# Kernel tuning notes

Measured on AMD Instinct MI355X. Metric: run time of the kernel, lower is better.

## Reference

```python
import jax, jax.numpy as jnp
import numpy as np

L = 8       # num decoder layers
S = 192     # seq_len = h*w = 24*8
D = 512     # d_model
DFF = 2048  # dim_feedforward
H, W, BS = 24, 8, 16
EPS = 1e-5


def setup_inputs() -> dict:
    key = jax.random.key(0)
    ks = jax.random.split(key, 8)
    f = jax.random.normal
    return {
        "q_feat": f(ks[0], (BS, D * L, H, W), jnp.float32),
        "g_feat": f(ks[1], (BS, D * L, H, W), jnp.float32),
        "targets": jax.random.randint(ks[2], (BS,), 0, 8),
        "score_embed": f(ks[3], (L, S, S), jnp.float32) * 0.05,
        "fc0_w": f(ks[4], (L, D, D), jnp.float32) * (1.0 / np.sqrt(D)),
        "fc0_b": jnp.zeros((L, D), jnp.float32),
        "bn1_g": jnp.ones((L,), jnp.float32),
        "bn1_b": jnp.zeros((L,), jnp.float32),
        "fc2_w": f(ks[5], (L, DFF, S), jnp.float32) * (1.0 / np.sqrt(S)),
        "fc2_b": jnp.zeros((L, DFF), jnp.float32),
        "bn2_g": jnp.ones((L, DFF), jnp.float32),
        "bn2_b": jnp.zeros((L, DFF), jnp.float32),
        "fc3_w": f(ks[6], (L, DFF), jnp.float32) * (1.0 / np.sqrt(DFF)),
        "fc3_b": jnp.zeros((L,), jnp.float32),
        "bn3_g": jnp.ones((L,), jnp.float32),
        "bn3_b": jnp.zeros((L,), jnp.float32),
    }


def _layer(qf, gf, se, w0, b0, g1, b1, w2, b2, g2, bb2, w3, b3, g3, bb3):
    # qf: [q,s,d], gf: [k,s,d]; shared fc0 projection for query and key
    query = jnp.einsum('qsd,ed->qse', qf, w0) + b0
    key_ = jnp.einsum('ksd,ed->kse', gf, w0) + b0
    # 4D correlation volume masked by sigmoid of learned score embedding
    score = jnp.einsum('qtd,ksd->qkst', query, key_) * jax.nn.sigmoid(se)
    q, k = score.shape[0], score.shape[1]
    sc = score.reshape(q * k, S, S)
    cat = jnp.concatenate([sc.max(axis=1), sc.max(axis=2)], axis=-1)  # [qk, 2S]
    x = cat.reshape(-1, S)  # [2qk, S]  (matches torch view(-1,1,S))
    # bn1: single channel -> normalize over all elements (training-mode BN)
    x = g1 * (x - x.mean()) * jax.lax.rsqrt(x.var() + EPS) + b1
    x = x @ w2.T + b2  # [2qk, DFF]
    mu = x.mean(0)
    var = x.var(0)
    x = g2 * (x - mu) * jax.lax.rsqrt(var + EPS) + bb2
    x = jax.nn.relu(x)
    x = x @ w3 + b3  # [2qk]
    x = x.reshape(-1, 2).sum(-1)  # [qk]: sum of row-max branch and col-max branch
    x = g3 * (x - x.mean()) * jax.lax.rsqrt(x.var() + EPS) + bb3
    return x.reshape(q, k)


def reference(q_feat, g_feat, targets, score_embed, fc0_w, fc0_b, bn1_g, bn1_b,
              fc2_w, fc2_b, bn2_g, bn2_b, fc3_w, fc3_b, bn3_g, bn3_b):
    bs = q_feat.shape[0]
    qf = jnp.transpose(q_feat, (0, 2, 3, 1)).reshape(bs, S, D * L)
    gf = jnp.transpose(g_feat, (0, 2, 3, 1)).reshape(bs, S, D * L)
    score = None
    for i in range(L):  # fixed small layer loop; each layer has distinct params
        si = _layer(qf[..., i * D:(i + 1) * D], gf[..., i * D:(i + 1) * D],
                    score_embed[i], fc0_w[i], fc0_b[i], bn1_g[i], bn1_b[i],
                    fc2_w[i], fc2_b[i], bn2_g[i], bn2_b[i],
                    fc3_w[i], fc3_b[i], bn3_g[i], bn3_b[i])
        score = si if score is None else score + si
    pair_labels = (targets[:, None] == targets[None, :]).astype(jnp.float32)
    return score, pair_labels
```

## Files before the change

kernel.cpp:

```cpp
#include <hip/hip_runtime.h>
#include <hip/hip_bf16.h>


#define EPS_ 1e-5f

typedef __attribute__((ext_vector_type(8))) _Float16 fp16x8;
typedef __attribute__((ext_vector_type(4)))  float   f32x4;
typedef __attribute__((ext_vector_type(16))) float   f32x16;

__device__ __forceinline__ unsigned fkey(float f) {
    unsigned u = __float_as_uint(f);
    return (u & 0x80000000u) ? ~u : (u | 0x80000000u);
}
__device__ __forceinline__ float funkey(unsigned k) {
    return (k & 0x80000000u) ? __uint_as_float(k & 0x7FFFFFFFu)
                             : __uint_as_float(~k);
}
__device__ __forceinline__ void gld16(const void* gp, void* lp) {
    __builtin_amdgcn_global_load_lds(
        (const __attribute__((address_space(1))) unsigned*)gp,
        (__attribute__((address_space(3))) unsigned*)lp, 16, 0, 0);
}

__global__ __launch_bounds__(256) void k_sig(const float* __restrict__ se,
                                             float* __restrict__ sig) {
    int i = blockIdx.x * 256 + threadIdx.x;
    float4 v = *(const float4*)(se + (size_t)i * 4);
    float4 o;
    o.x = 1.f / (1.f + __expf(-v.x));
    o.y = 1.f / (1.f + __expf(-v.y));
    o.z = 1.f / (1.f + __expf(-v.z));
    o.w = 1.f / (1.f + __expf(-v.w));
    *(float4*)(sig + (size_t)i * 4) = o;
}

__global__ __launch_bounds__(256) void k_fc0(const float* __restrict__ qfeat,
                                             const float* __restrict__ gfeat,
                                             const float* __restrict__ w0,
                                             const float* __restrict__ b0,
                                             _Float16* __restrict__ Qh) {
    int bid = blockIdx.x;
    int et = bid & 1;  bid >>= 1;
    int tt = bid % 3;  bid /= 3;
    int b  = bid & 15; bid >>= 4;
    int l  = bid & 7;  bid >>= 3;
    int sel = bid;
    const float* feat  = sel ? gfeat : qfeat;
    const float* Af = feat + (size_t)b * 4096 * 192 + (size_t)l * 512 * 192;
    const float* Wf = w0 + (size_t)l * 262144;
    int t0 = tt * 64, e0 = et * 256;

    __shared__ __align__(16) char At[64 * 80];
    __shared__ __align__(16) char Bt[256 * 80];

    int tid = threadIdx.x;
    int lane = tid & 63;
    int w = tid >> 6;
    int half = lane >> 5;
    int lrow = lane & 31;

    f32x16 acc[2][2];
    #pragma unroll
    for (int mi = 0; mi < 2; mi++)
        #pragma unroll
        for (int ni = 0; ni < 2; ni++)
            #pragma unroll
            for (int r = 0; r < 16; r++) acc[mi][ni][r] = 0.f;

    for (int d0 = 0; d0 < 512; d0 += 32) {
        __syncthreads();
        {
            int tA = tid & 63;
            int dp = tid >> 6;
            #pragma unroll
            for (int r = 0; r < 4; r++) {
                int d = dp * 2 + r * 8;
                float v0 = Af[(size_t)(d0 + d) * 192 + t0 + tA];
                float v1 = Af[(size_t)(d0 + d + 1) * 192 + t0 + tA];
                _Float16 h2[2] = {(_Float16)v0, (_Float16)v1};
                *(unsigned*)(At + tA * 80 + d * 2) = *(unsigned*)h2;
            }
        }
        {
            #pragma unroll
            for (int p = 0; p < 8; p++) {
                int s = tid + p * 256;
                int e = s >> 3;
                int q = s & 7;
                float4 wv = *(const float4*)(Wf + (size_t)(e0 + e) * 512 + d0 + q * 4);
                _Float16 h[4] = {(_Float16)wv.x, (_Float16)wv.y, (_Float16)wv.z, (_Float16)wv.w};
                *(uint2*)(Bt + e * 80 + q * 8) = *(uint2*)h;
            }
        }
        __syncthreads();
        #pragma unroll
        for (int ks = 0; ks < 2; ks++) {
            int koff = ks * 32 + half * 16;
            fp16x8 a[2], bf[2];
            #pragma unroll
            for (int mi = 0; mi < 2; mi++)
                a[mi] = *(const fp16x8*)(At + (mi * 32 + lrow) * 80 + koff);
            #pragma unroll
            for (int ni = 0; ni < 2; ni++)
                bf[ni] = *(const fp16x8*)(Bt + (w * 64 + ni * 32 + lrow) * 80 + koff);
            #pragma unroll
            for (int mi = 0; mi < 2; mi++)
                #pragma unroll
                for (int ni = 0; ni < 2; ni++)
                    acc[mi][ni] = __builtin_amdgcn_mfma_f32_32x32x16_f16(a[mi], bf[ni], acc[mi][ni], 0, 0, 0);
        }
    }

    _Float16* Obase = Qh + ((size_t)(sel * 8 + l) * 16 + b) * 98304;
    #pragma unroll
    for (int ni = 0; ni < 2; ni++) {
        int e = e0 + w * 64 + ni * 32 + lrow;
        float bias = b0[l * 512 + e];
        #pragma unroll
        for (int mi = 0; mi < 2; mi++) {
            #pragma unroll
            for (int r = 0; r < 16; r++) {
                int t = t0 + mi * 32 + (r & 3) + 8 * (r >> 2) + 4 * half;
                Obase[(size_t)t * 512 + e] = (_Float16)(acc[mi][ni][r] + bias);
            }
        }
    }
}

__global__ __launch_bounds__(256) void k_cvt(const float* __restrict__ src,
                                             _Float16* __restrict__ dst) {
    int i = blockIdx.x * 256 + threadIdx.x;
    float4 v = *(const float4*)(src + (size_t)i * 4);
    _Float16 h[4] = {(_Float16)v.x, (_Float16)v.y, (_Float16)v.z, (_Float16)v.w};
    *(uint2*)(dst + (size_t)i * 4) = *(uint2*)h;
}

__global__ __launch_bounds__(256) void k_score(const _Float16* __restrict__ Qh,
                                               const float* __restrict__ sig,
                                               unsigned* __restrict__ xkey) {
    int bid = blockIdx.x;
    int l = bid / 576;
    int rem = bid - l * 576;
    int grp = rem / 96;
    int within = rem - grp * 96;
    int mt = within >> 2;
    int nt = grp * 4 + (within & 3);
    int m0 = mt * 128, n0 = nt * 128;

    const char* Ag = (const char*)(Qh + (size_t)(8 + l) * 1572864);
    const char* Bg = (const char*)(Qh + (size_t)l * 1572864);
    const float* sg = sig + (size_t)l * 36864;

    __shared__ __align__(16) char As[8192];
    __shared__ __align__(16) char Bs[8192];
    __shared__ unsigned tmaxL[4][64];
    __shared__ unsigned smaxL[4][64];

    int tid = threadIdx.x;
    int lane = tid & 63;
    int w = tid >> 6;
    int wm = w >> 1, wn = w & 1;

    f32x4 acc[4][4];
    #pragma unroll
    for (int mi = 0; mi < 4; mi++)
        #pragma unroll
        for (int nj = 0; nj < 4; nj++)
            #pragma unroll
            for (int r = 0; r < 4; r++) acc[mi][nj][r] = 0.f;

    int srow = lane >> 2;
    int sseg = ((lane & 3) ^ ((srow >> 1) & 3)) * 16;
    int c = lane & 15;
    int kqp = (((lane >> 4) ^ ((c >> 1) & 3))) * 16;

    for (int d0 = 0; d0 < 1024; d0 += 64) {
        __syncthreads();
        #pragma unroll
        for (int j = 0; j < 2; j++) {
            int r = w * 32 + j * 16 + srow;
            gld16(Ag + (size_t)(m0 + r) * 1024 + d0 + sseg, As + (w * 32 + j * 16) * 64);
            gld16(Bg + (size_t)(n0 + r) * 1024 + d0 + sseg, Bs + (w * 32 + j * 16) * 64);
        }
        __syncthreads();
        fp16x8 a[4], b[4];
        #pragma unroll
        for (int mi = 0; mi < 4; mi++)
            a[mi] = *(const fp16x8*)(As + (wm * 64 + mi * 16 + c) * 64 + kqp);
        #pragma unroll
        for (int nj = 0; nj < 4; nj++)
            b[nj] = *(const fp16x8*)(Bs + (wn * 64 + nj * 16 + c) * 64 + kqp);
        #pragma unroll
        for (int mi = 0; mi < 4; mi++)
            #pragma unroll
            for (int nj = 0; nj < 4; nj++)
                acc[mi][nj] = __builtin_amdgcn_mfma_f32_16x16x32_f16(a[mi], b[nj], acc[mi][nj], 0, 0, 0);
    }

    int gmb = m0 + wm * 64;
    int kk = gmb / 192, sb = gmb - kk * 192;
    int gnb = n0 + wn * 64;
    int qq = gnb / 192, tb = gnb - qq * 192;
    int rq = (lane >> 4) * 4;

    float rowm[4][4];
    float colm[4];
    #pragma unroll
    for (int mi = 0; mi < 4; mi++)
        #pragma unroll
        for (int r = 0; r < 4; r++) rowm[mi][r] = -3.4e38f;
    #pragma unroll
    for (int nj = 0; nj < 4; nj++) colm[nj] = -3.4e38f;

    #pragma unroll
    for (int mi = 0; mi < 4; mi++) {
        #pragma unroll
        for (int r = 0; r < 4; r++) {
            int s = sb + mi * 16 + rq + r;
            const float* srow_p = sg + (size_t)s * 192 + tb;
            #pragma unroll
            for (int nj = 0; nj < 4; nj++) {
                float m = srow_p[nj * 16 + c];
                float v = acc[mi][nj][r] * m;
                rowm[mi][r] = fmaxf(rowm[mi][r], v);
                colm[nj] = fmaxf(colm[nj], v);
            }
        }
    }
    #pragma unroll
    for (int nj = 0; nj < 4; nj++) {
        colm[nj] = fmaxf(colm[nj], __shfl_xor(colm[nj], 16));
        colm[nj] = fmaxf(colm[nj], __shfl_xor(colm[nj], 32));
    }
    if (lane < 16) {
        #pragma unroll
        for (int nj = 0; nj < 4; nj++)
            tmaxL[wm * 2 + wn][nj * 16 + lane] = fkey(colm[nj]);
    }
    #pragma unroll
    for (int st = 1; st <= 8; st <<= 1)
        #pragma unroll
        for (int mi = 0; mi < 4; mi++)
            #pragma unroll
            for (int r = 0; r < 4; r++)
                rowm[mi][r] = fmaxf(rowm[mi][r], __shfl_xor(rowm[mi][r], st));
    if (c == 0) {
        #pragma unroll
        for (int mi = 0; mi < 4; mi++)
            #pragma unroll
            for (int r = 0; r < 4; r++)
                smaxL[wm * 2 + wn][mi * 16 + rq + r] = fkey(rowm[mi][r]);
    }
    __syncthreads();

    #pragma unroll
    for (int rep = 0; rep < 2; rep++) {
        int idx = tid + rep * 256;
        int wp = idx >> 7;
        int which = (idx >> 6) & 1;
        int off = idx & 63;
        int wmf = wp >> 1, wnf = wp & 1;
        int kf = (m0 + wmf * 64) / 192, sbf = (m0 + wmf * 64) % 192;
        int qf = (n0 + wnf * 64) / 192, tbf = (n0 + wnf * 64) % 192;
        int jp = qf * 16 + kf;
        if (which == 0)
            atomicMax(&xkey[((size_t)l * 512 + 2 * jp) * 192 + tbf + off], tmaxL[wp][off]);
        else
            atomicMax(&xkey[((size_t)l * 512 + 2 * jp + 1) * 192 + sbf + off], smaxL[wp][off]);
    }
}

__global__ __launch_bounds__(256) void k_bn1s(const unsigned* __restrict__ xkey,
                                              float* __restrict__ bn1acc) {
    int l = blockIdx.x / 48;
    int b = blockIdx.x - l * 48;
    const unsigned* xk = xkey + (size_t)l * 98304 + b * 2048;
    int tid = threadIdx.x;
    uint4 v1 = *(const uint4*)(xk + tid * 8);
    uint4 v2 = *(const uint4*)(xk + tid * 8 + 4);
    float s = 0.f, s2 = 0.f;
    float e;
    e = funkey(v1.x); s += e; s2 += e * e;
    e = funkey(v1.y); s += e; s2 += e * e;
    e = funkey(v1.z); s += e; s2 += e * e;
    e = funkey(v1.w); s += e; s2 += e * e;
    e = funkey(v2.x); s += e; s2 += e * e;
    e = funkey(v2.y); s += e; s2 += e * e;
    e = funkey(v2.z); s += e; s2 += e * e;
    e = funkey(v2.w); s += e; s2 += e * e;
    #pragma unroll
    for (int o = 32; o; o >>= 1) { s += __shfl_down(s, o); s2 += __shfl_down(s2, o); }
    if ((tid & 63) == 0) {
        atomicAdd(&bn1acc[l * 2], s);
        atomicAdd(&bn1acc[l * 2 + 1], s2);
    }
}

__global__ __launch_bounds__(256) void k_bn1n(const unsigned* __restrict__ xkey,
                                              const float* __restrict__ bn1acc,
                                              const float* __restrict__ g1,
                                              const float* __restrict__ b1,
                                              _Float16* __restrict__ xh) {
    int idx = blockIdx.x * 256 + threadIdx.x;
    int l = idx / 24576;
    float mu = bn1acc[l * 2] * (1.f / 98304.f);
    float var = bn1acc[l * 2 + 1] * (1.f / 98304.f) - mu * mu;
    float a1 = g1[l] * rsqrtf(var + EPS_);
    float c1 = b1[l] - mu * a1;
    uint4 kv = *(const uint4*)(xkey + (size_t)idx * 4);
    _Float16 h[4];
    h[0] = (_Float16)(funkey(kv.x) * a1 + c1);
    h[1] = (_Float16)(funkey(kv.y) * a1 + c1);
    h[2] = (_Float16)(funkey(kv.z) * a1 + c1);
    h[3] = (_Float16)(funkey(kv.w) * a1 + c1);
    *(uint2*)(xh + (size_t)idx * 4) = *(uint2*)h;
}

__global__ __launch_bounds__(256) void k_fc2(const _Float16* __restrict__ xh,
                                             const _Float16* __restrict__ w2h,
                                             const float* __restrict__ b2,
                                             _Float16* __restrict__ hb,
                                             float* __restrict__ bn2sum,
                                             float* __restrict__ bn2sq) {
    int bid = blockIdx.x;
    int l = bid >> 6;
    int rem = bid & 63;
    int mt = rem & 3, nt = rem >> 2;
    int m0 = mt * 128, n0 = nt * 128;
    const char* Ag = (const char*)(xh + (size_t)l * 98304);
    const char* Bg = (const char*)(w2h + (size_t)l * 393216);

    __shared__ __align__(16) char As[8192];
    __shared__ __align__(16) char Bs[8192];

    int tid = threadIdx.x;
    int lane = tid & 63;
    int w = tid >> 6;
    int wm = w >> 1, wn = w & 1;

    f32x4 acc[4][4];
    #pragma unroll
    for (int mi = 0; mi < 4; mi++)
        #pragma unroll
        for (int nj = 0; nj < 4; nj++)
            #pragma unroll
            for (int r = 0; r < 4; r++) acc[mi][nj][r] = 0.f;

    int srow = lane >> 2;
    int sseg = ((lane & 3) ^ ((srow >> 1) & 3)) * 16;
    int c = lane & 15;
    int kqp = (((lane >> 4) ^ ((c >> 1) & 3))) * 16;

    for (int d0 = 0; d0 < 384; d0 += 64) {
        __syncthreads();
        #pragma unroll
        for (int j = 0; j < 2; j++) {
            int r = w * 32 + j * 16 + srow;
            gld16(Ag + (size_t)(m0 + r) * 384 + d0 + sseg, As + (w * 32 + j * 16) * 64);
            gld16(Bg + (size_t)(n0 + r) * 384 + d0 + sseg, Bs + (w * 32 + j * 16) * 64);
        }
        __syncthreads();
        fp16x8 a[4], b[4];
        #pragma unroll
        for (int mi = 0; mi < 4; mi++)
            a[mi] = *(const fp16x8*)(As + (wm * 64 + mi * 16 + c) * 64 + kqp);
        #pragma unroll
        for (int nj = 0; nj < 4; nj++)
            b[nj] = *(const fp16x8*)(Bs + (wn * 64 + nj * 16 + c) * 64 + kqp);
        #pragma unroll
        for (int mi = 0; mi < 4; mi++)
            #pragma unroll
            for (int nj = 0; nj < 4; nj++)
                acc[mi][nj] = __builtin_amdgcn_mfma_f32_16x16x32_f16(a[mi], b[nj], acc[mi][nj], 0, 0, 0);
    }

    int rq = (lane >> 4) * 4;
    _Float16* ho = hb + (size_t)l * 1048576;
    float colsum[4], colsq[4];
    #pragma unroll
    for (int nj = 0; nj < 4; nj++) { colsum[nj] = 0.f; colsq[nj] = 0.f; }
    #pragma unroll
    for (int nj = 0; nj < 4; nj++) {
        int gf = n0 + wn * 64 + nj * 16 + c;
        float bias = b2[l * 2048 + gf];
        #pragma unroll
        for (int mi = 0; mi < 4; mi++) {
            #pragma unroll
            for (int r = 0; r < 4; r++) {
                int gm = m0 + wm * 64 + mi * 16 + rq + r;
                float v = acc[mi][nj][r] + bias;
                ho[(size_t)gm * 2048 + gf] = (_Float16)v;
                colsum[nj] += v;
                colsq[nj] += v * v;
            }
        }
    }
    #pragma unroll
    for (int nj = 0; nj < 4; nj++) {
        colsum[nj] += __shfl_xor(colsum[nj], 16);
        colsum[nj] += __shfl_xor(colsum[nj], 32);
        colsq[nj]  += __shfl_xor(colsq[nj], 16);
        colsq[nj]  += __shfl_xor(colsq[nj], 32);
    }
    if (lane < 16) {
        #pragma unroll
        for (int nj = 0; nj < 4; nj++) {
            int gf = n0 + wn * 64 + nj * 16 + lane;
            atomicAdd(&bn2sum[l * 2048 + gf], colsum[nj]);
            atomicAdd(&bn2sq[l * 2048 + gf], colsq[nj]);
        }
    }
}

__global__ __launch_bounds__(256) void k_fc3(const _Float16* __restrict__ hb,
                                             const float* __restrict__ bn2sum,
                                             const float* __restrict__ bn2sq,
                                             const float* __restrict__ g2,
                                             const float* __restrict__ bb2,
                                             const float* __restrict__ w3,
                                             const float* __restrict__ b3,
                                             float* __restrict__ ybuf) {
    int n = blockIdx.x & 511;
    int l = blockIdx.x >> 9;
    const _Float16* h = hb + ((size_t)l * 512 + n) * 2048;
    int tid = threadIdx.x;
    int f0 = tid * 8;
    fp16x8 hv = *(const fp16x8*)(h + f0);
    float sum = 0.f;
    #pragma unroll
    for (int j = 0; j < 8; j++) {
        int f = f0 + j;
        float mu = bn2sum[l * 2048 + f] * (1.f / 512.f);
        float var = bn2sq[l * 2048 + f] * (1.f / 512.f) - mu * mu;
        float a2 = g2[l * 2048 + f] * rsqrtf(var + EPS_);
        float c2 = bb2[l * 2048 + f] - mu * a2;
        float v = (float)hv[j] * a2 + c2;
        v = fmaxf(v, 0.f);
        sum += v * w3[l * 2048 + f];
    }
    __shared__ float red[4];
    int lane = tid & 63, w = tid >> 6;
    #pragma unroll
    for (int o = 32; o; o >>= 1) sum += __shfl_down(sum, o);
    if (lane == 0) red[w] = sum;
    __syncthreads();
    if (tid == 0) ybuf[l * 512 + n] = red[0] + red[1] + red[2] + red[3] + b3[l];
}

__global__ __launch_bounds__(256) void k_final(const float* __restrict__ ybuf,
                                               const float* __restrict__ g3,
                                               const float* __restrict__ bb3,
                                               const int* __restrict__ targets,
                                               float* __restrict__ out) {
    int tid = threadIdx.x;
    __shared__ float red[8];
    float scoreacc = 0.f;
    for (int l = 0; l < 8; l++) {
        float z = ybuf[l * 512 + 2 * tid] + ybuf[l * 512 + 2 * tid + 1];
        float s = z, s2 = z * z;
        int lane = tid & 63, w = tid >> 6;
        #pragma unroll
        for (int o = 32; o; o >>= 1) { s += __shfl_down(s, o); s2 += __shfl_down(s2, o); }
        if (lane == 0) { red[w] = s; red[4 + w] = s2; }
        __syncthreads();
        float S1 = red[0] + red[1] + red[2] + red[3];
        float S2 = red[4] + red[5] + red[6] + red[7];
        float mu = S1 * (1.f / 256.f);
        float var = S2 * (1.f / 256.f) - mu * mu;
        float rstd = rsqrtf(var + EPS_);
        scoreacc += g3[l] * (z - mu) * rstd + bb3[l];
        __syncthreads();
    }
    out[tid] = scoreacc;
    int i = tid >> 4, j = tid & 15;
    out[256 + tid] = (targets[i] == targets[j]) ? 1.f : 0.f;
}

extern "C" void kernel_launch(void* const* d_in, const int* in_sizes, int n_in,
                              void* d_out, int out_size, void* d_ws, size_t ws_size,
                              hipStream_t stream) {
    const float* q_feat = (const float*)d_in[0];
    const float* g_feat = (const float*)d_in[1];
    const int*   targets = (const int*)d_in[2];
    const float* se     = (const float*)d_in[3];
    const float* fc0_w  = (const float*)d_in[4];
    const float* fc0_b  = (const float*)d_in[5];
    const float* bn1_g  = (const float*)d_in[6];
    const float* bn1_b  = (const float*)d_in[7];
    const float* fc2_w  = (const float*)d_in[8];
    const float* fc2_b  = (const float*)d_in[9];
    const float* bn2_g  = (const float*)d_in[10];
    const float* bn2_b  = (const float*)d_in[11];
    const float* fc3_w  = (const float*)d_in[12];
    const float* fc3_b  = (const float*)d_in[13];
    const float* bn3_g  = (const float*)d_in[14];
    const float* bn3_b  = (const float*)d_in[15];

    float* ws = (float*)d_ws;
    _Float16* Qh   = (_Float16*)ws;
    float*    sig  = ws + 12582912;
    unsigned* xkey = (unsigned*)(ws + 12877824);
    _Float16* xh   = (_Float16*)(ws + 13664256);
    _Float16* w2h  = (_Float16*)(ws + 14057472);
    _Float16* hb   = (_Float16*)(ws + 15630336);
    float* bn2sum = ws + 19824640;
    float* bn2sq  = ws + 19841024;
    float* bn1acc = ws + 19857408;
    float* ybuf   = ws + 19857424;
    float* out  = (float*)d_out;

    hipMemsetAsync(xkey, 0, 786432 * sizeof(unsigned), stream);
    hipMemsetAsync(bn2sum, 0, (2 * 16384 + 16) * sizeof(float), stream);
    k_sig<<<288, 256, 0, stream>>>(se, sig);
    k_cvt<<<3072, 256, 0, stream>>>(fc2_w, w2h);
    k_fc0<<<1536, 256, 0, stream>>>(q_feat, g_feat, fc0_w, fc0_b, Qh);
    k_score<<<4608, 256, 0, stream>>>(Qh, sig, xkey);
    k_bn1s<<<384, 256, 0, stream>>>(xkey, bn1acc);
    k_bn1n<<<768, 256, 0, stream>>>(xkey, bn1acc, bn1_g, bn1_b, xh);
    k_fc2<<<512, 256, 0, stream>>>(xh, w2h, fc2_b, hb, bn2sum, bn2sq);
    k_fc3<<<4096, 256, 0, stream>>>(hb, bn2sum, bn2sq, bn2_g, bn2_b, fc3_w, fc3_b, ybuf);
    k_final<<<1, 256, 0, stream>>>(ybuf, bn3_g, bn3_b, targets, out);
}
```

Baseline: 428.7 us.

## Split fc0 into transpose plus LDS-direct GEMM, enlarge score tile, precompute BN2 table

Replaces the fused fc0 kernel with a transpose-to-fp16 kernel and a GEMM that uses global_load_lds async loads, with fc0 weights pre-converted to fp16. The score GEMM tile grows from 128x128 to 256x128, halving block count and reusing B fragments across more rows, with restructured max reductions and atomics. Also adjusts the LDS swizzle, moves the BN2 memset later, and adds a prep kernel that precomputes per-feature BN2 scale/shift/w3 so fc3 does less math. This adds launches and extra buffers, and the larger tile raises register pressure.

After: 488.7 us. 14.0% more time.

```diff
diff --git a/kernel.cpp b/kernel.cpp
--- a/kernel.cpp
+++ b/kernel.cpp
@@ -34,99 +34,6 @@
     *(float4*)(sig + (size_t)i * 4) = o;
 }
 
-__global__ __launch_bounds__(256) void k_fc0(const float* __restrict__ qfeat,
-                                             const float* __restrict__ gfeat,
-                                             const float* __restrict__ w0,
-                                             const float* __restrict__ b0,
-                                             _Float16* __restrict__ Qh) {
-    int bid = blockIdx.x;
-    int et = bid & 1;  bid >>= 1;
-    int tt = bid % 3;  bid /= 3;
-    int b  = bid & 15; bid >>= 4;
-    int l  = bid & 7;  bid >>= 3;
-    int sel = bid;
-    const float* feat  = sel ? gfeat : qfeat;
-    const float* Af = feat + (size_t)b * 4096 * 192 + (size_t)l * 512 * 192;
-    const float* Wf = w0 + (size_t)l * 262144;
-    int t0 = tt * 64, e0 = et * 256;
-
-    __shared__ __align__(16) char At[64 * 80];
-    __shared__ __align__(16) char Bt[256 * 80];
-
-    int tid = threadIdx.x;
-    int lane = tid & 63;
-    int w = tid >> 6;
-    int half = lane >> 5;
-    int lrow = lane & 31;
-
-    f32x16 acc[2][2];
-    #pragma unroll
-    for (int mi = 0; mi < 2; mi++)
-        #pragma unroll
-        for (int ni = 0; ni < 2; ni++)
-            #pragma unroll
-            for (int r = 0; r < 16; r++) acc[mi][ni][r] = 0.f;
-
-    for (int d0 = 0; d0 < 512; d0 += 32) {
-        __syncthreads();
-        {
-            int tA = tid & 63;
-            int dp = tid >> 6;
-            #pragma unroll
-            for (int r = 0; r < 4; r++) {
-                int d = dp * 2 + r * 8;
-                float v0 = Af[(size_t)(d0 + d) * 192 + t0 + tA];
-                float v1 = Af[(size_t)(d0 + d + 1) * 192 + t0 + tA];
-                _Float16 h2[2] = {(_Float16)v0, (_Float16)v1};
-                *(unsigned*)(At + tA * 80 + d * 2) = *(unsigned*)h2;
-            }
-        }
-        {
-            #pragma unroll
-            for (int p = 0; p < 8; p++) {
-                int s = tid + p * 256;
-                int e = s >> 3;
-                int q = s & 7;
-                float4 wv = *(const float4*)(Wf + (size_t)(e0 + e) * 512 + d0 + q * 4);
-                _Float16 h[4] = {(_Float16)wv.x, (_Float16)wv.y, (_Float16)wv.z, (_Float16)wv.w};
-                *(uint2*)(Bt + e * 80 + q * 8) = *(uint2*)h;
-            }
-        }
-        __syncthreads();
-        #pragma unroll
-        for (int ks = 0; ks < 2; ks++) {
-            int koff = ks * 32 + half * 16;
-            fp16x8 a[2], bf[2];
-            #pragma unroll
-            for (int mi = 0; mi < 2; mi++)
-                a[mi] = *(const fp16x8*)(At + (mi * 32 + lrow) * 80 + koff);
-            #pragma unroll
-            for (int ni = 0; ni < 2; ni++)
-                bf[ni] = *(const fp16x8*)(Bt + (w * 64 + ni * 32 + lrow) * 80 + koff);
-            #pragma unroll
-            for (int mi = 0; mi < 2; mi++)
-                #pragma unroll
-                for (int ni = 0; ni < 2; ni++)
-                    acc[mi][ni] = __builtin_amdgcn_mfma_f32_32x32x16_f16(a[mi], bf[ni], acc[mi][ni], 0, 0, 0);
-        }
-    }
-
-    _Float16* Obase = Qh + ((size_t)(sel * 8 + l) * 16 + b) * 98304;
-    #pragma unroll
-    for (int ni = 0; ni < 2; ni++) {
-        int e = e0 + w * 64 + ni * 32 + lrow;
-        float bias = b0[l * 512 + e];
-        #pragma unroll
-        for (int mi = 0; mi < 2; mi++) {
-            #pragma unroll
-            for (int r = 0; r < 16; r++) {
-                int t = t0 + mi * 32 + (r & 3) + 8 * (r >> 2) + 4 * half;
-                Obase[(size_t)t * 512 + e] = (_Float16)(acc[mi][ni][r] + bias);
-            }
-        }
-    }
-}
-
 __global__ __launch_bounds__(256) void k_cvt(const float* __restrict__ src,
                                              _Float16* __restrict__ dst) {
     int i = blockIdx.x * 256 + threadIdx.x;
@@ -135,138 +42,261 @@
     *(uint2*)(dst + (size_t)i * 4) = *(uint2*)h;
 }
 
+__global__ __launch_bounds__(256) void k_tr(const float* __restrict__ qfeat,
+                                            const float* __restrict__ gfeat,
+                                            _Float16* __restrict__ fT) {
+    int bid = blockIdx.x;
+    int dc = bid & 3;  bid >>= 2;
+    int b  = bid & 15; bid >>= 4;
+    int l  = bid & 7;  bid >>= 3;
+    int sel = bid;
+    const float* feat = (sel ? gfeat : qfeat) + (size_t)b * 786432 + (size_t)(l * 512 + dc * 128) * 192;
+
+    __shared__ __align__(16) char T[192 * 272];
+    int tid = threadIdx.x;
+    int tl = tid & 63;
+    int dg = tid >> 6;
+
+    #pragma unroll
+    for (int ds = 0; ds < 16; ds++) {
+        int d = ds * 8 + dg * 2;
+        #pragma unroll
+        for (int ts = 0; ts < 3; ts++) {
+            int t = ts * 64 + tl;
+            float v0 = feat[(size_t)d * 192 + t];
+            float v1 = feat[(size_t)(d + 1) * 192 + t];
+            _Float16 h2[2] = {(_Float16)v0, (_Float16)v1};
+            *(unsigned*)(T + t * 272 + d * 2) = *(unsigned*)h2;
+        }
+    }
+    __syncthreads();
+    _Float16* ob = fT + (size_t)(sel * 8 + l) * 1572864 + (size_t)b * 98304 + dc * 128;
+    #pragma unroll
+    for (int ws = 0; ws < 12; ws++) {
+        int flat = ws * 256 + tid;
+        int row = flat >> 4;
+        int ch = flat & 15;
+        uint4 v = *(const uint4*)(T + row * 272 + ch * 16);
+        *(uint4*)(ob + (size_t)row * 512 + ch * 8) = v;
+    }
+}
+
+__global__ __launch_bounds__(256) void k_fc0g(const _Float16* __restrict__ fT,
+                                              const _Float16* __restrict__ w0h,
+                                              const float* __restrict__ b0,
+                                              _Float16* __restrict__ Qh) {
+    int bid = blockIdx.x;
+    int sl = bid / 96;
+    int rem = bid - sl * 96;
+    int mt = rem >> 2, nt = rem & 3;
+    int m0 = mt * 128, n0 = nt * 128;
+    int l = sl & 7;
+    const char* Ag = (const char*)(fT + (size_t)sl * 1572864);
+    const char* Bg = (const char*)(w0h + (size_t)l * 262144);
+
+    __shared__ __align__(16) char As[8192];
+    __shared__ __align__(16) char Bs[8192];
+
+    int tid = threadIdx.x;
+    int lane = tid & 63;
+    int w = tid >> 6;
+    int wm = w >> 1, wn = w & 1;
+
+    f32x4 acc[4][4];
+    #pragma unroll
+    for (int mi = 0; mi < 4; mi++)
+        #pragma unroll
+        for (int nj = 0; nj < 4; nj++)
+            #pragma unroll
+            for (int r = 0; r < 4; r++) acc[mi][nj][r] = 0.f;
+
+    int srow = lane >> 2;
+    int sseg = ((lane & 3) ^ ((lane >> 3) & 3)) * 16;
+    int c = lane & 15;
+    int kqp = (((lane >> 4) ^ ((c >> 1) & 3))) * 16;
+
+    for (int d0 = 0; d0 < 1024; d0 += 64) {
+        __syncthreads();
+        #pragma unroll
+        for (int j = 0; j < 2; j++) {
+            int r = w * 32 + j * 16 + srow;
+            gld16(Ag + (size_t)(m0 + r) * 1024 + d0 + sseg, As + (w * 32 + j * 16) * 64);
+            gld16(Bg + (size_t)(n0 + r) * 1024 + d0 + sseg, Bs + (w * 32 + j * 16) * 64);
+        }
+        __syncthreads();
+        fp16x8 a[4], b[4];
+        #pragma unroll
+        for (int mi = 0; mi < 4; mi++)
+            a[mi] = *(const fp16x8*)(As + (wm * 64 + mi * 16 + c) * 64 + kqp);
+        #pragma unroll
+        for (int nj = 0; nj < 4; nj++)
+            b[nj] = *(const fp16x8*)(Bs + (wn * 64 + nj * 16 + c) * 64 + kqp);
+        #pragma unroll
+        for (int mi = 0; mi < 4; mi++)
+            #pragma unroll
+            for (int nj = 0; nj < 4; nj++)
+                acc[mi][nj] = __builtin_amdgcn_mfma_f32_16x16x32_f16(a[mi], b[nj], acc[mi][nj], 0, 0, 0);
+    }
+
+    int rq = (lane >> 4) * 4;
+    _Float16* ob = Qh + (size_t)sl * 1572864;
+    #pragma unroll
+    for (int nj = 0; nj < 4; nj++) {
+        int e = n0 + wn * 64 + nj * 16 + c;
+        float bias = b0[l * 512 + e];
+        #pragma unroll
+        for (int mi = 0; mi < 4; mi++) {
+            #pragma unroll
+            for (int r = 0; r < 4; r++) {
+                int m = m0 + wm * 64 + mi * 16 + rq + r;
+                ob[(size_t)m * 512 + e] = (_Float16)(acc[mi][nj][r] + bias);
+            }
+        }
+    }
+}
+
 __global__ __launch_bounds__(256) void k_score(const _Float16* __restrict__ Qh,
                                                const float* __restrict__ sig,
                                                unsigned* __restrict__ xkey) {
     int bid = blockIdx.x;
-    int l = bid / 576;
-    int rem = bid - l * 576;
-    int grp = rem / 96;
-    int within = rem - grp * 96;
+    int l = bid / 288;
+    int rem = bid - l * 288;
+    int grp = rem / 48;
+    int within = rem - grp * 48;
     int mt = within >> 2;
     int nt = grp * 4 + (within & 3);
-    int m0 = mt * 128, n0 = nt * 128;
+    int m0 = mt * 256, n0 = nt * 128;
 
     const char* Ag = (const char*)(Qh + (size_t)(8 + l) * 1572864);
     const char* Bg = (const char*)(Qh + (size_t)l * 1572864);
     const float* sg = sig + (size_t)l * 36864;
 
-    __shared__ __align__(16) char As[8192];
+    __shared__ __align__(16) char As[16384];
     __shared__ __align__(16) char Bs[8192];
-    __shared__ unsigned tmaxL[4][64];
-    __shared__ unsigned smaxL[4][64];
+    __shared__ unsigned tmax[4][128];
+    __shared__ unsigned smax[2][256];
 
     int tid = threadIdx.x;
     int lane = tid & 63;
     int w = tid >> 6;
     int wm = w >> 1, wn = w & 1;
 
-    f32x4 acc[4][4];
-    #pragma unroll
-    for (int mi = 0; mi < 4; mi++)
+    f32x4 acc[8][4];
+    #pragma unroll
+    for (int mi = 0; mi < 8; mi++)
         #pragma unroll
         for (int nj = 0; nj < 4; nj++)
             #pragma unroll
             for (int r = 0; r < 4; r++) acc[mi][nj][r] = 0.f;
 
     int srow = lane >> 2;
-    int sseg = ((lane & 3) ^ ((srow >> 1) & 3)) * 16;
+    int sseg = ((lane & 3) ^ ((lane >> 3) & 3)) * 16;
     int c = lane & 15;
     int kqp = (((lane >> 4) ^ ((c >> 1) & 3))) * 16;
 
     for (int d0 = 0; d0 < 1024; d0 += 64) {
         __syncthreads();
         #pragma unroll
+        for (int j = 0; j < 4; j++) {
+            int r = w * 64 + j * 16 + srow;
+            gld16(Ag + (size_t)(m0 + r) * 1024 + d0 + sseg, As + (w * 64 + j * 16) * 64);
+        }
+        #pragma unroll
         for (int j = 0; j < 2; j++) {
             int r = w * 32 + j * 16 + srow;
-            gld16(Ag + (size_t)(m0 + r) * 1024 + d0 + sseg, As + (w * 32 + j * 16) * 64);
             gld16(Bg + (size_t)(n0 + r) * 1024 + d0 + sseg, Bs + (w * 32 + j * 16) * 64);
         }
         __syncthreads();
-        fp16x8 a[4], b[4];
-        #pragma unroll
-        for (int mi = 0; mi < 4; mi++)
-            a[mi] = *(const fp16x8*)(As + (wm * 64 + mi * 16 + c) * 64 + kqp);
+        fp16x8 b[4];
         #pragma unroll
         for (int nj = 0; nj < 4; nj++)
             b[nj] = *(const fp16x8*)(Bs + (wn * 64 + nj * 16 + c) * 64 + kqp);
         #pragma unroll
-        for (int mi = 0; mi < 4; mi++)
+        for (int mi = 0; mi < 8; mi++) {
+            fp16x8 a = *(const fp16x8*)(As + (wm * 128 + mi * 16 + c) * 64 + kqp);
             #pragma unroll
             for (int nj = 0; nj < 4; nj++)
-                acc[mi][nj] = __builtin_amdgcn_mfma_f32_16x16x32_f16(a[mi], b[nj], acc[mi][nj], 0, 0, 0);
-    }
-
-    int gmb = m0 + wm * 64;
-    int kk = gmb / 192, sb = gmb - kk * 192;
-    int gnb = n0 + wn * 64;
-    int qq = gnb / 192, tb = gnb - qq * 192;
+                acc[mi][nj] = __builtin_amdgcn_mfma_f32_16x16x32_f16(a, b[nj], acc[mi][nj], 0, 0, 0);
+        }
+    }
+
+    int sb_w = m0 + wm * 128;
+    int tb_w = (n0 + wn * 64) % 192;
     int rq = (lane >> 4) * 4;
 
-    float rowm[4][4];
-    float colm[4];
-    #pragma unroll
-    for (int mi = 0; mi < 4; mi++)
+    float rowm[8][4];
+    float colm[2][4];
+    #pragma unroll
+    for (int mi = 0; mi < 8; mi++)
         #pragma unroll
         for (int r = 0; r < 4; r++) rowm[mi][r] = -3.4e38f;
     #pragma unroll
-    for (int nj = 0; nj < 4; nj++) colm[nj] = -3.4e38f;
-
-    #pragma unroll
-    for (int mi = 0; mi < 4; mi++) {
+    for (int g = 0; g < 2; g++)
+        #pragma unroll
+        for (int nj = 0; nj < 4; nj++) colm[g][nj] = -3.4e38f;
+
+    #pragma unroll
+    for (int mi = 0; mi < 8; mi++) {
+        int g = mi >> 2;
+        int sRow = (sb_w + mi * 16) % 192;
         #pragma unroll
         for (int r = 0; r < 4; r++) {
-            int s = sb + mi * 16 + rq + r;
-            const float* srow_p = sg + (size_t)s * 192 + tb;
+            int s = sRow + rq + r;
+            const float* sp = sg + (size_t)s * 192 + tb_w;
             #pragma unroll
             for (int nj = 0; nj < 4; nj++) {
-                float m = srow_p[nj * 16 + c];
+                float m = sp[nj * 16 + c];
                 float v = acc[mi][nj][r] * m;
                 rowm[mi][r] = fmaxf(rowm[mi][r], v);
-                colm[nj] = fmaxf(colm[nj], v);
+                colm[g][nj] = fmaxf(colm[g][nj], v);
             }
         }
     }
     #pragma unroll
-    for (int nj = 0; nj < 4; nj++) {
-        colm[nj] = fmaxf(colm[nj], __shfl_xor(colm[nj], 16));
-        colm[nj] = fmaxf(colm[nj], __shfl_xor(colm[nj], 32));
-    }
+    for (int g = 0; g < 2; g++)
+        #pragma unroll
+        for (int nj = 0; nj < 4; nj++) {
+            colm[g][nj] = fmaxf(colm[g][nj], __shfl_xor(colm[g][nj], 16));
+            colm[g][nj] = fmaxf(colm[g][nj], __shfl_xor(colm[g][nj], 32));
+        }
     if (lane < 16) {
         #pragma unroll
-        for (int nj = 0; nj < 4; nj++)
-            tmaxL[wm * 2 + wn][nj * 16 + lane] = fkey(colm[nj]);
+        for (int g = 0; g < 2; g++)
+            #pragma unroll
+            for (int nj = 0; nj < 4; nj++)
+                tmax[wm * 2 + g][wn * 64 + nj * 16 + lane] = fkey(colm[g][nj]);
     }
     #pragma unroll
     for (int st = 1; st <= 8; st <<= 1)
         #pragma unroll
-        for (int mi = 0; mi < 4; mi++)
+        for (int mi = 0; mi < 8; mi++)
             #pragma unroll
             for (int r = 0; r < 4; r++)
                 rowm[mi][r] = fmaxf(rowm[mi][r], __shfl_xor(rowm[mi][r], st));
     if (c == 0) {
         #pragma unroll
-        for (int mi = 0; mi < 4; mi++)
+        for (int mi = 0; mi < 8; mi++)
             #pragma unroll
             for (int r = 0; r < 4; r++)
-                smaxL[wm * 2 + wn][mi * 16 + rq + r] = fkey(rowm[mi][r]);
+                smax[wn][wm * 128 + mi * 16 + rq + r] = fkey(rowm[mi][r]);
     }
     __syncthreads();
 
     #pragma unroll
-    for (int rep = 0; rep < 2; rep++) {
+    for (int rep = 0; rep < 4; rep++) {
         int idx = tid + rep * 256;
-        int wp = idx >> 7;
-        int which = (idx >> 6) & 1;
-        int off = idx & 63;
-        int wmf = wp >> 1, wnf = wp & 1;
-        int kf = (m0 + wmf * 64) / 192, sbf = (m0 + wmf * 64) % 192;
-        int qf = (n0 + wnf * 64) / 192, tbf = (n0 + wnf * 64) % 192;
-        int jp = qf * 16 + kf;
-        if (which == 0)
-            atomicMax(&xkey[((size_t)l * 512 + 2 * jp) * 192 + tbf + off], tmaxL[wp][off]);
-        else
-            atomicMax(&xkey[((size_t)l * 512 + 2 * jp + 1) * 192 + sbf + off], smaxL[wp][off]);
+        if (idx < 512) {
+            int g = idx >> 7, col = idx & 127;
+            int kk = (m0 + g * 64) / 192;
+            int q = (n0 + col) / 192, t = (n0 + col) % 192;
+            atomicMax(&xkey[((size_t)l * 512 + 2 * (q * 16 + kk)) * 192 + t], tmax[g][col]);
+        } else {
+            int i2 = idx - 512;
+            int wnf = i2 >> 8, row = i2 & 255;
+            int q = (n0 + wnf * 64) / 192;
+            int kk = (m0 + row) / 192, s = (m0 + row) % 192;
+            atomicMax(&xkey[((size_t)l * 512 + 2 * (q * 16 + kk) + 1) * 192 + s], smax[wnf][row]);
+        }
     }
 }
 
@@ -347,7 +377,7 @@
             for (int r = 0; r < 4; r++) acc[mi][nj][r] = 0.f;
 
     int srow = lane >> 2;
-    int sseg = ((lane & 3) ^ ((srow >> 1) & 3)) * 16;
+    int sseg = ((lane & 3) ^ ((lane >> 3) & 3)) * 16;
     int c = lane & 15;
     int kqp = (((lane >> 4) ^ ((c >> 1) & 3))) * 16;
 
@@ -412,12 +442,22 @@
     }
 }
 
+__global__ __launch_bounds__(256) void k_prep(const float* __restrict__ bn2sum,
+                                              const float* __restrict__ bn2sq,
+                                              const float* __restrict__ g2,
+                                              const float* __restrict__ bb2,
+                                              const float* __restrict__ w3,
+                                              float4* __restrict__ tbl) {
+    int i = blockIdx.x * 256 + threadIdx.x;
+    float mu = bn2sum[i] * (1.f / 512.f);
+    float var = bn2sq[i] * (1.f / 512.f) - mu * mu;
+    float a2 = g2[i] * rsqrtf(var + EPS_);
+    float c2 = bb2[i] - mu * a2;
+    tbl[i] = make_float4(a2, c2, w3[i], 0.f);
+}
+
 __global__ __launch_bounds__(256) void k_fc3(const _Float16* __restrict__ hb,
-                                             const float* __restrict__ bn2sum,
-                                             const float* __restrict__ bn2sq,
-                                             const float* __restrict__ g2,
-                                             const float* __restrict__ bb2,
-                                             const float* __restrict__ w3,
+                                             const float4* __restrict__ tbl,
                                              const float* __restrict__ b3,
                                              float* __restrict__ ybuf) {
     int n = blockIdx.x & 511;
@@ -426,17 +466,14 @@
     int tid = threadIdx.x;
     int f0 = tid * 8;
     fp16x8 hv = *(const fp16x8*)(h + f0);
+    const float4* tb = tbl + l * 2048 + f0;
     float sum = 0.f;
     #pragma unroll
     for (int j = 0; j < 8; j++) {
-        int f = f0 + j;
-        float mu = bn2sum[l * 2048 + f] * (1.f / 512.f);
-        float var = bn2sq[l * 2048 + f] * (1.f / 512.f) - mu * mu;
-        float a2 = g2[l * 2048 + f] * rsqrtf(var + EPS_);
-        float c2 = bb2[l * 2048 + f] - mu * a2;
-        float v = (float)hv[j] * a2 + c2;
+        float4 p = tb[j];
+        float v = fmaf((float)hv[j], p.x, p.y);
         v = fmaxf(v, 0.f);
-        sum += v * w3[l * 2048 + f];
+        sum += v * p.z;
     }
     __shared__ float red[4];
     int lane = tid & 63, w = tid >> 6;
@@ -500,24 +537,30 @@
     _Float16* Qh   = (_Float16*)ws;
     float*    sig  = ws + 12582912;
     unsigned* xkey = (unsigned*)(ws + 12877824);
-    _Float16* xh   = (_Float16*)(ws + 13664256);
-    _Float16* w2h  = (_Float16*)(ws + 14057472);
-    _Float16* hb   = (_Float16*)(ws + 15630336);
-    float* bn2sum = ws + 19824640;
-    float* bn2sq  = ws + 19841024;
-    float* bn1acc = ws + 19857408;
-    float* ybuf   = ws + 19857424;
+    _Float16* w0h  = (_Float16*)(ws + 13664256);
+    _Float16* fT   = (_Float16*)(ws + 14712832);
+    _Float16* xh   = (_Float16*)(ws + 14712832);
+    _Float16* w2h  = (_Float16*)(ws + 15106048);
+    _Float16* hb   = (_Float16*)(ws + 16678912);
+    float* bn2sum = ws + 20873216;
+    float* bn2sq  = ws + 20889600;
+    float* bn1acc = ws + 20905984;
+    float* ybuf   = ws + 20906000;
+    float4* tbl   = (float4*)(ws + 20910096);
     float* out  = (float*)d_out;
 
     hipMemsetAsync(xkey, 0, 786432 * sizeof(unsigned), stream);
-    hipMemsetAsync(bn2sum, 0, (2 * 16384 + 16) * sizeof(float), stream);
     k_sig<<<288, 256, 0, stream>>>(se, sig);
+    k_cvt<<<2048, 256, 0, stream>>>(fc0_w, w0h);
+    k_tr<<<1024, 256, 0, stream>>>(q_feat, g_feat, fT);
+    k_fc0g<<<1536, 256, 0, stream>>>(fT, w0h, fc0_b, Qh);
     k_cvt<<<3072, 256, 0, stream>>>(fc2_w, w2h);
-    k_fc0<<<1536, 256, 0, stream>>>(q_feat, g_feat, fc0_w, fc0_b, Qh);
-    k_score<<<4608, 256, 0, stream>>>(Qh, sig, xkey);
+    k_score<<<2304, 256, 0, stream>>>(Qh, sig, xkey);
+    hipMemsetAsync(bn2sum, 0, 32784 * sizeof(float), stream);
     k_bn1s<<<384, 256, 0, stream>>>(xkey, bn1acc);
     k_bn1n<<<768, 256, 0, stream>>>(xkey, bn1acc, bn1_g, bn1_b, xh);
     k_fc2<<<512, 256, 0, stream>>>(xh, w2h, fc2_b, hb, bn2sum, bn2sq);
-    k_fc3<<<4096, 256, 0, stream>>>(hb, bn2sum, bn2sq, bn2_g, bn2_b, fc3_w, fc3_b, ybuf);
+    k_prep<<<64, 256, 0, stream>>>(bn2sum, bn2sq, bn2_g, bn2_b, fc3_w, tbl);
+    k_fc3<<<4096, 256, 0, stream>>>(hb, tbl, fc3_b, ybuf);
     k_final<<<1, 256, 0, stream>>>(ybuf, bn3_g, bn3_b, targets, out);
 }
```
